# Kernel optimization log

Hardware: AMD Instinct MI355X
Metric: run time of the kernel (lower is better)

Reference implementation:

```python
import jax, jax.numpy as jnp
import numpy as np

N_EMBD = 2560
N_HEAD = 32
HEAD_DIM = N_EMBD // N_HEAD  # 80
ROTARY_DIM = 32
SEQ = 2048
BSZ = 1


def _rope_tables(seq_len, rotary_dim, base=10000.0):
    inv_freq = 1.0 / (base ** (np.arange(0, rotary_dim, 2, dtype=np.float32) / rotary_dim))
    t = np.arange(seq_len, dtype=np.float32)
    freqs = np.outer(t, inv_freq)                      # [S, rd/2]
    emb = np.concatenate([freqs, freqs], axis=-1)      # [S, rd]
    return jnp.asarray(np.cos(emb)), jnp.asarray(np.sin(emb))


def setup_inputs() -> dict:
    key = jax.random.key(0)
    k1, k2, k3, k4, k5 = jax.random.split(key, 5)
    op_size = HEAD_DIM * (N_HEAD + 2 * N_HEAD)  # fused q,k,v => 3*n_embd
    hidden_states = jax.random.normal(k1, (BSZ, SEQ, N_EMBD), dtype=jnp.float32)
    Wqkv_w = jax.random.normal(k2, (op_size, N_EMBD), dtype=jnp.float32) * 0.02
    Wqkv_b = jax.random.normal(k3, (op_size,), dtype=jnp.float32) * 0.02
    out_w = jax.random.normal(k4, (N_EMBD, N_EMBD), dtype=jnp.float32) * 0.02
    out_b = jax.random.normal(k5, (N_EMBD,), dtype=jnp.float32) * 0.02
    cos, sin = _rope_tables(SEQ, ROTARY_DIM)
    return {"hidden_states": hidden_states, "Wqkv_w": Wqkv_w, "Wqkv_b": Wqkv_b,
            "out_w": out_w, "out_b": out_b, "cos": cos, "sin": sin}


def apply_partial_rotary(x, cos, sin):
    # x: [S, B, H, D]; cos/sin: [S, rd]
    rd = cos.shape[-1]
    c = cos[:, None, None, :]
    s = sin[:, None, None, :]
    x_rot = x[..., :rd]
    # NOTE: faithful to source -- rotated half is concatenated WITHOUT negation
    tmp = jnp.concatenate([x[..., rd // 2:rd], x[..., :rd // 2]], axis=-1)
    rotten = x_rot * c + tmp * s
    return jnp.concatenate([rotten, x[..., rd:]], axis=-1)


def reference(hidden_states, Wqkv_w, Wqkv_b, out_w, out_b, cos, sin):
    bsz, q_len, _ = hidden_states.shape
    qkv = hidden_states @ Wqkv_w.T + Wqkv_b            # [B, S, 3*E]
    q, k, v = jnp.split(qkv, 3, axis=-1)
    # [B, S, H, D] -> [S, B, H, D] for rotary
    q = q.reshape(bsz, q_len, N_HEAD, HEAD_DIM).transpose(1, 0, 2, 3)
    k = k.reshape(bsz, q_len, N_HEAD, HEAD_DIM).transpose(1, 0, 2, 3)
    v = v.reshape(bsz, q_len, N_HEAD, HEAD_DIM).transpose(0, 2, 1, 3)  # [B, H, S, D]
    cos_t, sin_t = cos[:q_len], sin[:q_len]
    q = apply_partial_rotary(q, cos_t, sin_t).transpose(1, 2, 0, 3)    # [B, H, S, D]
    k = apply_partial_rotary(k, cos_t, sin_t).transpose(1, 2, 0, 3)    # [B, H, S, D]
    scale = 1.0 / jnp.sqrt(jnp.asarray(HEAD_DIM, dtype=q.dtype))
    scores = jnp.einsum('bhqd,bhkd->bhqk', q, k) * scale
    causal = jnp.tril(jnp.ones((q_len, q_len), dtype=bool))
    scores = jnp.where(causal, scores, jnp.asarray(-1e30, dtype=scores.dtype))
    probs = jax.nn.softmax(scores, axis=-1)
    out = jnp.einsum('bhqk,bhkd->bhqd', probs, v)       # [B, H, S, D]
    out = out.transpose(0, 2, 1, 3).reshape(bsz, q_len, N_EMBD)
    return out @ out_w.T + out_b
```

## Files before the change

### kernel.cpp

```cpp
#include <hip/hip_runtime.h>
#include <cstdint>
#include <cstddef>

typedef unsigned short bf16_t;
typedef __attribute__((ext_vector_type(8))) short bf16x8;
typedef __attribute__((ext_vector_type(4))) float f32x4;

__device__ __forceinline__ float bf2f(bf16_t b) {
  unsigned int u = ((unsigned int)b) << 16;
  return __builtin_bit_cast(float, u);
}
__device__ __forceinline__ bf16_t f2bf(float f) {
  unsigned int u = __builtin_bit_cast(unsigned int, f);
  u += 0x7fffu + ((u >> 16) & 1u);
  return (bf16_t)(u >> 16);
}
__device__ __forceinline__ float lo16(unsigned int u) { return __builtin_bit_cast(float, u << 16); }
__device__ __forceinline__ float hi16(unsigned int u) { return __builtin_bit_cast(float, u & 0xffff0000u); }

constexpr int SEQ = 2048, NE = 2560, NH = 32, HD = 80, OP = 7680;

__global__ void cvt_f32_bf16(const float* __restrict__ s, bf16_t* __restrict__ d) {
  const int t = blockIdx.x * 256 + threadIdx.x;
  float4 v = ((const float4*)s)[t];
  ushort4 o;
  o.x = f2bf(v.x); o.y = f2bf(v.y); o.z = f2bf(v.z); o.w = f2bf(v.w);
  ((ushort4*)d)[t] = o;
}

__device__ __forceinline__ void store_out(bf16_t* p, float v) { *p = f2bf(v); }
__device__ __forceinline__ void store_out(float* p, float v)  { *p = v; }

template <typename OutT>
__global__ __launch_bounds__(256, 2) void gemm_bt_bias(
    const bf16_t* __restrict__ A,
    const bf16_t* __restrict__ B,
    const float*  __restrict__ bias,
    OutT* __restrict__ C,
    int M, int N, int K)
{
  __shared__ bf16_t As[128 * 32];
  __shared__ bf16_t Bs[128 * 32];

  const int tid  = threadIdx.x;
  const int lane = tid & 63;
  const int wave = tid >> 6;
  const int m0 = blockIdx.y * 128;
  const int n0 = blockIdx.x * 128;
  const int mw = (wave >> 1) * 64;
  const int nw = (wave & 1) * 64;
  const int lm = lane & 15;
  const int lq = lane >> 4;

  f32x4 acc[4][4];
#pragma unroll
  for (int i = 0; i < 4; ++i)
#pragma unroll
    for (int j = 0; j < 4; ++j)
      acc[i][j] = (f32x4){0.f, 0.f, 0.f, 0.f};

  const int ldr = lane >> 2;
  const int ldc = (lane & 3) * 8;

  for (int kt = 0; kt < K; kt += 32) {
#pragma unroll
    for (int r = 0; r < 2; ++r) {
      const int seg = wave * 2 + r;
      const int row = seg * 16 + ldr;
      const bf16_t* ga = A + (size_t)(m0 + row) * K + kt + ldc;
      const bf16_t* gb = B + (size_t)(n0 + row) * K + kt + ldc;
      __builtin_amdgcn_global_load_lds(
          (const __attribute__((address_space(1))) unsigned int*)ga,
          (__attribute__((address_space(3))) unsigned int*)&As[seg * 512], 16, 0, 0);
      __builtin_amdgcn_global_load_lds(
          (const __attribute__((address_space(1))) unsigned int*)gb,
          (__attribute__((address_space(3))) unsigned int*)&Bs[seg * 512], 16, 0, 0);
    }
    __syncthreads();

    bf16x8 af[4], bfq[4];
#pragma unroll
    for (int i = 0; i < 4; ++i)
      af[i] = *(const bf16x8*)&As[(mw + i * 16 + lm) * 32 + lq * 8];
#pragma unroll
    for (int j = 0; j < 4; ++j)
      bfq[j] = *(const bf16x8*)&Bs[(nw + j * 16 + lm) * 32 + lq * 8];

#pragma unroll
    for (int i = 0; i < 4; ++i)
#pragma unroll
      for (int j = 0; j < 4; ++j)
        acc[i][j] = __builtin_amdgcn_mfma_f32_16x16x32_bf16(af[i], bfq[j], acc[i][j], 0, 0, 0);

    __syncthreads();
  }

#pragma unroll
  for (int i = 0; i < 4; ++i) {
#pragma unroll
    for (int j = 0; j < 4; ++j) {
      const int n = n0 + nw + j * 16 + lm;
      const float bv = bias[n];
#pragma unroll
      for (int r = 0; r < 4; ++r) {
        const int m = m0 + mw + i * 16 + lq * 4 + r;
        store_out(&C[(size_t)m * N + n], acc[i][j][r] + bv);
      }
    }
  }
}

__global__ void rope_kernel(bf16_t* __restrict__ qkv,
                            const float* __restrict__ cosb,
                            const float* __restrict__ sinb)
{
  const int t = blockIdx.x * 256 + threadIdx.x;
  const int i  = t & 15;
  const int qk = (t >> 4) & 1;
  const int h  = (t >> 5) & 31;
  const int s  = t >> 10;
  const size_t base = (size_t)s * OP + qk * NE + h * HD;
  const float xi = bf2f(qkv[base + i]);
  const float xj = bf2f(qkv[base + i + 16]);
  const float c1 = cosb[s * 32 + i];
  const float s1 = sinb[s * 32 + i];
  const float c2 = cosb[s * 32 + i + 16];
  const float s2 = sinb[s * 32 + i + 16];
  qkv[base + i]      = f2bf(xi * c1 + xj * s1);
  qkv[base + i + 16] = f2bf(xj * c2 + xi * s2);
}

constexpr int KSTR = 96;
constexpr int VSTR = 72;
constexpr int PSTR = 72;

__global__ __launch_bounds__(256, 2) void attn_mfma(
    const bf16_t* __restrict__ qkv, bf16_t* __restrict__ aout)
{
  __shared__ bf16_t Ks[64 * KSTR];
  __shared__ bf16_t Vt[80 * VSTR];
  __shared__ bf16_t Ps[4][32 * PSTR];

  const int h    = blockIdx.y;
  const int qt   = (int)gridDim.x - 1 - blockIdx.x;
  const int q0   = qt * 128;
  const int tid  = threadIdx.x;
  const int lane = tid & 63;
  const int wave = tid >> 6;
  const int lm   = lane & 15;
  const int quad = lane >> 4;

  const int jb0 = 16 * wave;
  const int jb1 = 64 + 16 * wave;
  const int qg0 = q0 + jb0 + lm;
  const int qg1 = q0 + jb1 + lm;

  const int koff = NE + h * HD;
  const int voff = 2 * NE + h * HD;
  const float SC = 0.1118033988749895f;

  bf16x8 qf[2][3];
  {
    const bf16_t* q_r0 = qkv + (size_t)qg0 * OP + h * HD;
    const bf16_t* q_r1 = qkv + (size_t)qg1 * OP + h * HD;
#pragma unroll
    for (int ks = 0; ks < 3; ++ks) {
      const int col = ks * 32 + quad * 8;
      if (col < 80) {
        qf[0][ks] = *(const bf16x8*)(q_r0 + col);
        qf[1][ks] = *(const bf16x8*)(q_r1 + col);
      } else {
        qf[0][ks] = (bf16x8){0,0,0,0,0,0,0,0};
        qf[1][ks] = (bf16x8){0,0,0,0,0,0,0,0};
      }
    }
  }

  int kofs[3];
#pragma unroll
  for (int r = 0; r < 3; ++r) {
    const int e = (wave * 3 + r) * 512 + lane * 8;
    const int row = e / 96, c = e % 96;
    kofs[r] = row * OP + (c < 80 ? c : c - 16);
  }

  const int vp = tid & 31;
  const int vg = tid >> 5;

  f32x4 oacc[5][2];
#pragma unroll
  for (int mt = 0; mt < 5; ++mt) {
    oacc[mt][0] = (f32x4){0.f,0.f,0.f,0.f};
    oacc[mt][1] = (f32x4){0.f,0.f,0.f,0.f};
  }
  float lsum0 = 0.f, lsum1 = 0.f;

  const int ntiles = 2 * qt + 2;
  for (int t = 0; t < ntiles; ++t) {
    const int kb = t * 64;

#pragma unroll
    for (int r = 0; r < 3; ++r) {
      const bf16_t* g = qkv + (size_t)kb * OP + koff + kofs[r];
      __builtin_amdgcn_global_load_lds(
          (const __attribute__((address_space(1))) unsigned int*)g,
          (__attribute__((address_space(3))) unsigned int*)&Ks[(wave * 3 + r) * 512],
          16, 0, 0);
    }
    {
      const bf16_t* va = qkv + (size_t)(kb + 2 * vp) * OP + voff + vg * 10;
      const bf16_t* vb = va + OP;
      unsigned int wa[5], wb[5];
#pragma unroll
      for (int j = 0; j < 5; ++j) {
        wa[j] = *(const unsigned int*)(va + 2 * j);
        wb[j] = *(const unsigned int*)(vb + 2 * j);
      }
#pragma unroll
      for (int tt = 0; tt < 10; ++tt) {
        const unsigned int A = wa[tt >> 1], B = wb[tt >> 1];
        const unsigned int pk = (tt & 1) ? ((A >> 16) | (B & 0xffff0000u))
                                         : ((A & 0xffffu) | (B << 16));
        *(unsigned int*)&Vt[(vg * 10 + tt) * VSTR + 2 * vp] = pk;
      }
    }
    __syncthreads();

    f32x4 sacc[4][2];
#pragma unroll
    for (int mt = 0; mt < 4; ++mt) {
      sacc[mt][0] = (f32x4){0.f,0.f,0.f,0.f};
      sacc[mt][1] = (f32x4){0.f,0.f,0.f,0.f};
    }
#pragma unroll
    for (int ks = 0; ks < 3; ++ks) {
      bf16x8 kf[4];
#pragma unroll
      for (int mt = 0; mt < 4; ++mt)
        kf[mt] = *(const bf16x8*)&Ks[(mt * 16 + lm) * KSTR + ks * 32 + quad * 8];
#pragma unroll
      for (int mt = 0; mt < 4; ++mt) {
        sacc[mt][0] = __builtin_amdgcn_mfma_f32_16x16x32_bf16(kf[mt], qf[0][ks], sacc[mt][0], 0, 0, 0);
        sacc[mt][1] = __builtin_amdgcn_mfma_f32_16x16x32_bf16(kf[mt], qf[1][ks], sacc[mt][1], 0, 0, 0);
      }
    }

    const int keyb = kb + quad * 4;
#pragma unroll
    for (int mt = 0; mt < 4; ++mt) {
#pragma unroll
      for (int nt = 0; nt < 2; ++nt) {
        const int qg = nt ? qg1 : qg0;
        float ps[4];
#pragma unroll
        for (int r = 0; r < 4; ++r) {
          float p = __expf(sacc[mt][nt][r] * SC);
          p = (keyb + mt * 16 + r > qg) ? 0.f : p;
          ps[r] = p;
        }
        if (nt == 0) lsum0 += (ps[0] + ps[1]) + (ps[2] + ps[3]);
        else         lsum1 += (ps[0] + ps[1]) + (ps[2] + ps[3]);
        ushort4 pk;
        pk.x = f2bf(ps[0]); pk.y = f2bf(ps[1]); pk.z = f2bf(ps[2]); pk.w = f2bf(ps[3]);
        *(ushort4*)&Ps[wave][((nt ? jb1 - 64 + 16 : jb0) , (nt * 16 + lm)) * 0 + (nt * 16 + lm) * PSTR + mt * 16 + quad * 4] = pk;
      }
    }

#pragma unroll
    for (int ks = 0; ks < 2; ++ks) {
      bf16x8 vf[5], pf0, pf1;
#pragma unroll
      for (int mt = 0; mt < 5; ++mt)
        vf[mt] = *(const bf16x8*)&Vt[(mt * 16 + lm) * VSTR + ks * 32 + quad * 8];
      pf0 = *(const bf16x8*)&Ps[wave][(0 * 16 + lm) * PSTR + ks * 32 + quad * 8];
      pf1 = *(const bf16x8*)&Ps[wave][(1 * 16 + lm) * PSTR + ks * 32 + quad * 8];
#pragma unroll
      for (int mt = 0; mt < 5; ++mt) {
        oacc[mt][0] = __builtin_amdgcn_mfma_f32_16x16x32_bf16(vf[mt], pf0, oacc[mt][0], 0, 0, 0);
        oacc[mt][1] = __builtin_amdgcn_mfma_f32_16x16x32_bf16(vf[mt], pf1, oacc[mt][1], 0, 0, 0);
      }
    }
    __syncthreads();
  }

  lsum0 += __shfl_xor(lsum0, 16); lsum0 += __shfl_xor(lsum0, 32);
  lsum1 += __shfl_xor(lsum1, 16); lsum1 += __shfl_xor(lsum1, 32);
  const float inv0 = 1.f / lsum0, inv1 = 1.f / lsum1;
#pragma unroll
  for (int nt = 0; nt < 2; ++nt) {
    const int qrow = nt ? qg1 : qg0;
    const float inv = nt ? inv1 : inv0;
    bf16_t* base = aout + (size_t)qrow * NE + h * HD + quad * 4;
#pragma unroll
    for (int mt = 0; mt < 5; ++mt) {
      ushort4 st;
      st.x = f2bf(oacc[mt][nt][0] * inv);
      st.y = f2bf(oacc[mt][nt][1] * inv);
      st.z = f2bf(oacc[mt][nt][2] * inv);
      st.w = f2bf(oacc[mt][nt][3] * inv);
      *(ushort4*)(base + mt * 16) = st;
    }
  }
}

extern "C" void kernel_launch(void* const* d_in, const int* in_sizes, int n_in,
                              void* d_out, int out_size, void* d_ws, size_t ws_size,
                              hipStream_t stream)
{
  const float* hs   = (const float*)d_in[0];
  const float* wqkv = (const float*)d_in[1];
  const float* bqkv = (const float*)d_in[2];
  const float* wout = (const float*)d_in[3];
  const float* bout = (const float*)d_in[4];
  const float* cosb = (const float*)d_in[5];
  const float* sinb = (const float*)d_in[6];

  bf16_t* hs_bf   = (bf16_t*)d_ws;
  bf16_t* wqkv_bf = hs_bf   + (size_t)SEQ * NE;
  bf16_t* wout_bf = wqkv_bf + (size_t)OP * NE;
  bf16_t* qkv     = wout_bf + (size_t)NE * NE;
  bf16_t* aout    = qkv     + (size_t)SEQ * OP;
  float*  out     = (float*)d_out;

  cvt_f32_bf16<<<(SEQ * NE) / 1024, 256, 0, stream>>>(hs,   hs_bf);
  cvt_f32_bf16<<<(OP * NE)  / 1024, 256, 0, stream>>>(wqkv, wqkv_bf);
  cvt_f32_bf16<<<(NE * NE)  / 1024, 256, 0, stream>>>(wout, wout_bf);

  gemm_bt_bias<bf16_t><<<dim3(OP / 128, SEQ / 128), 256, 0, stream>>>(
      hs_bf, wqkv_bf, bqkv, qkv, SEQ, OP, NE);
  rope_kernel<<<(SEQ * NH * 2 * 16) / 256, 256, 0, stream>>>(qkv, cosb, sinb);
  attn_mfma<<<dim3(SEQ / 128, NH), 256, 0, stream>>>(qkv, aout);
  gemm_bt_bias<float><<<dim3(NE / 128, SEQ / 128), 256, 0, stream>>>(
      aout, wout_bf, bout, out, SEQ, NE, NE);
}
```

Baseline: 432.5 us.

## Pad GEMM and attention LDS tiles, merge conversion kernels, raise GEMM occupancy

The GEMM shared-memory tiles get a padded row stride of 40, and the async global-to-LDS loads are remapped to fill that padded layout, with half the waves loading A and half loading B. The goal is to cut LDS bank conflicts on the MFMA fragment reads. GEMM launch bounds go from 2 to 3 blocks per SM. The attention K tile stride is padded to 104 with a matching load remap, and the three fp32-to-bf16 conversion launches become one kernel. The padded layouts rely on the tricky load-to-LDS address mapping, and the extra padding columns are filled with duplicate data.

```diff
diff --git a/kernel.cpp b/kernel.cpp
--- a/kernel.cpp
+++ b/kernel.cpp
@@ -15,13 +15,19 @@
   u += 0x7fffu + ((u >> 16) & 1u);
   return (bf16_t)(u >> 16);
 }
-__device__ __forceinline__ float lo16(unsigned int u) { return __builtin_bit_cast(float, u << 16); }
-__device__ __forceinline__ float hi16(unsigned int u) { return __builtin_bit_cast(float, u & 0xffff0000u); }
 
 constexpr int SEQ = 2048, NE = 2560, NH = 32, HD = 80, OP = 7680;
 
-__global__ void cvt_f32_bf16(const float* __restrict__ s, bf16_t* __restrict__ d) {
-  const int t = blockIdx.x * 256 + threadIdx.x;
+__global__ void cvt3(const float* __restrict__ s0, const float* __restrict__ s1,
+                     const float* __restrict__ s2, bf16_t* __restrict__ d0,
+                     bf16_t* __restrict__ d1, bf16_t* __restrict__ d2)
+{
+  constexpr int N0 = SEQ * NE / 4, N1 = OP * NE / 4, N2 = NE * NE / 4;
+  int t = blockIdx.x * 256 + threadIdx.x;
+  const float* s; bf16_t* d;
+  if (t < N0)            { s = s0; d = d0; }
+  else if (t < N0 + N1)  { s = s1; d = d1; t -= N0; }
+  else                   { s = s2; d = d2; t -= N0 + N1; }
   float4 v = ((const float4*)s)[t];
   ushort4 o;
   o.x = f2bf(v.x); o.y = f2bf(v.y); o.z = f2bf(v.z); o.w = f2bf(v.w);
@@ -31,16 +37,18 @@
 __device__ __forceinline__ void store_out(bf16_t* p, float v) { *p = f2bf(v); }
 __device__ __forceinline__ void store_out(float* p, float v)  { *p = v; }
 
+constexpr int GSTR = 40;
+
 template <typename OutT>
-__global__ __launch_bounds__(256, 2) void gemm_bt_bias(
+__global__ __launch_bounds__(256, 3) void gemm_bt_bias(
     const bf16_t* __restrict__ A,
     const bf16_t* __restrict__ B,
     const float*  __restrict__ bias,
     OutT* __restrict__ C,
     int M, int N, int K)
 {
-  __shared__ bf16_t As[128 * 32];
-  __shared__ bf16_t Bs[128 * 32];
+  __shared__ bf16_t As[128 * GSTR];
+  __shared__ bf16_t Bs[128 * GSTR];
 
   const int tid  = threadIdx.x;
   const int lane = tid & 63;
@@ -59,32 +67,38 @@
     for (int j = 0; j < 4; ++j)
       acc[i][j] = (f32x4){0.f, 0.f, 0.f, 0.f};
 
-  const int ldr = lane >> 2;
-  const int ldc = (lane & 3) * 8;
+  const bf16_t* gsrc = (wave < 2) ? A : B;
+  bf16_t* lbase      = (wave < 2) ? As : Bs;
+  const size_t rowbase = (size_t)((wave < 2) ? m0 : n0) * K;
+  int gofs[5], lofs[5];
+#pragma unroll
+  for (int r = 0; r < 5; ++r) {
+    const int ci  = (wave & 1) * 5 + r;
+    const int c   = ci * 64 + lane;
+    const int row = c / 5;
+    const int cc  = c % 5;
+    const int col = (cc < 4) ? cc * 8 : 0;
+    gofs[r] = row * K + col;
+    lofs[r] = ci * 512;
+  }
 
   for (int kt = 0; kt < K; kt += 32) {
 #pragma unroll
-    for (int r = 0; r < 2; ++r) {
-      const int seg = wave * 2 + r;
-      const int row = seg * 16 + ldr;
-      const bf16_t* ga = A + (size_t)(m0 + row) * K + kt + ldc;
-      const bf16_t* gb = B + (size_t)(n0 + row) * K + kt + ldc;
+    for (int r = 0; r < 5; ++r) {
+      const bf16_t* g = gsrc + rowbase + kt + gofs[r];
       __builtin_amdgcn_global_load_lds(
-          (const __attribute__((address_space(1))) unsigned int*)ga,
-          (__attribute__((address_space(3))) unsigned int*)&As[seg * 512], 16, 0, 0);
-      __builtin_amdgcn_global_load_lds(
-          (const __attribute__((address_space(1))) unsigned int*)gb,
-          (__attribute__((address_space(3))) unsigned int*)&Bs[seg * 512], 16, 0, 0);
+          (const __attribute__((address_space(1))) unsigned int*)g,
+          (__attribute__((address_space(3))) unsigned int*)&lbase[lofs[r]], 16, 0, 0);
     }
     __syncthreads();
 
     bf16x8 af[4], bfq[4];
 #pragma unroll
     for (int i = 0; i < 4; ++i)
-      af[i] = *(const bf16x8*)&As[(mw + i * 16 + lm) * 32 + lq * 8];
+      af[i] = *(const bf16x8*)&As[(mw + i * 16 + lm) * GSTR + lq * 8];
 #pragma unroll
     for (int j = 0; j < 4; ++j)
-      bfq[j] = *(const bf16x8*)&Bs[(nw + j * 16 + lm) * 32 + lq * 8];
+      bfq[j] = *(const bf16x8*)&Bs[(nw + j * 16 + lm) * GSTR + lq * 8];
 
 #pragma unroll
     for (int i = 0; i < 4; ++i)
@@ -130,7 +144,7 @@
   qkv[base + i + 16] = f2bf(xj * c2 + xi * s2);
 }
 
-constexpr int KSTR = 96;
+constexpr int KSTR = 104;
 constexpr int VSTR = 72;
 constexpr int PSTR = 72;
 
@@ -176,12 +190,18 @@
     }
   }
 
-  int kofs[3];
-#pragma unroll
-  for (int r = 0; r < 3; ++r) {
-    const int e = (wave * 3 + r) * 512 + lane * 8;
-    const int row = e / 96, c = e % 96;
-    kofs[r] = row * OP + (c < 80 ? c : c - 16);
+  int kofs[4], klds[4];
+  bool kact[4];
+#pragma unroll
+  for (int r = 0; r < 4; ++r) {
+    const int seg = wave * 4 + r;
+    kact[r] = (seg < 13);
+    const int c   = (seg < 13 ? seg : 0) * 64 + lane;
+    const int row = c / 13;
+    const int cc  = c % 13;
+    const int col = (cc < 10) ? cc * 8 : (cc - 10) * 8;
+    kofs[r] = row * OP + col;
+    klds[r] = (seg < 13 ? seg : 0) * 512;
   }
 
   const int vp = tid & 31;
@@ -200,12 +220,13 @@
     const int kb = t * 64;
 
 #pragma unroll
-    for (int r = 0; r < 3; ++r) {
-      const bf16_t* g = qkv + (size_t)kb * OP + koff + kofs[r];
-      __builtin_amdgcn_global_load_lds(
-          (const __attribute__((address_space(1))) unsigned int*)g,
-          (__attribute__((address_space(3))) unsigned int*)&Ks[(wave * 3 + r) * 512],
-          16, 0, 0);
+    for (int r = 0; r < 4; ++r) {
+      if (kact[r]) {
+        const bf16_t* g = qkv + (size_t)kb * OP + koff + kofs[r];
+        __builtin_amdgcn_global_load_lds(
+            (const __attribute__((address_space(1))) unsigned int*)g,
+            (__attribute__((address_space(3))) unsigned int*)&Ks[klds[r]], 16, 0, 0);
+      }
     }
     {
       const bf16_t* va = qkv + (size_t)(kb + 2 * vp) * OP + voff + vg * 10;
@@ -262,7 +283,7 @@
         else         lsum1 += (ps[0] + ps[1]) + (ps[2] + ps[3]);
         ushort4 pk;
         pk.x = f2bf(ps[0]); pk.y = f2bf(ps[1]); pk.z = f2bf(ps[2]); pk.w = f2bf(ps[3]);
-        *(ushort4*)&Ps[wave][((nt ? jb1 - 64 + 16 : jb0) , (nt * 16 + lm)) * 0 + (nt * 16 + lm) * PSTR + mt * 16 + quad * 4] = pk;
+        *(ushort4*)&Ps[wave][(nt * 16 + lm) * PSTR + mt * 16 + quad * 4] = pk;
       }
     }
 
@@ -322,9 +343,8 @@
   bf16_t* aout    = qkv     + (size_t)SEQ * OP;
   float*  out     = (float*)d_out;
 
-  cvt_f32_bf16<<<(SEQ * NE) / 1024, 256, 0, stream>>>(hs,   hs_bf);
-  cvt_f32_bf16<<<(OP * NE)  / 1024, 256, 0, stream>>>(wqkv, wqkv_bf);
-  cvt_f32_bf16<<<(NE * NE)  / 1024, 256, 0, stream>>>(wout, wout_bf);
+  constexpr int CVT_T = (SEQ * NE + OP * NE + NE * NE) / 4;
+  cvt3<<<CVT_T / 256, 256, 0, stream>>>(hs, wqkv, wout, hs_bf, wqkv_bf, wout_bf);
 
   gemm_bt_bias<bf16_t><<<dim3(OP / 128, SEQ / 128), 256, 0, stream>>>(
       hs_bf, wqkv_bf, bqkv, qkv, SEQ, OP, NE);
```

After: 440.3 us. No clear change (+1.8%).

## Halve attention query tile to 64 rows and merge conversion launches

Applied to the files above, without the earlier changes.

The attention kernel now gives each block 64 query rows instead of 128, so each wave handles one 16-row query fragment. That doubles the grid, cuts register and LDS use, and raises the occupancy hint to 4 blocks per CU. The intent is better occupancy and load balance across the causal triangle, at the cost of loading each K/V tile twice as often per head. The three f32-to-bf16 conversion kernels are also merged into one launch to cut launch overhead.

```diff
diff --git a/kernel.cpp b/kernel.cpp
--- a/kernel.cpp
+++ b/kernel.cpp
@@ -15,13 +15,19 @@
   u += 0x7fffu + ((u >> 16) & 1u);
   return (bf16_t)(u >> 16);
 }
-__device__ __forceinline__ float lo16(unsigned int u) { return __builtin_bit_cast(float, u << 16); }
-__device__ __forceinline__ float hi16(unsigned int u) { return __builtin_bit_cast(float, u & 0xffff0000u); }
 
 constexpr int SEQ = 2048, NE = 2560, NH = 32, HD = 80, OP = 7680;
 
-__global__ void cvt_f32_bf16(const float* __restrict__ s, bf16_t* __restrict__ d) {
-  const int t = blockIdx.x * 256 + threadIdx.x;
+__global__ void cvt3(const float* __restrict__ s0, const float* __restrict__ s1,
+                     const float* __restrict__ s2, bf16_t* __restrict__ d0,
+                     bf16_t* __restrict__ d1, bf16_t* __restrict__ d2)
+{
+  constexpr int N0 = SEQ * NE / 4, N1 = OP * NE / 4;
+  int t = blockIdx.x * 256 + threadIdx.x;
+  const float* s; bf16_t* d;
+  if (t < N0)            { s = s0; d = d0; }
+  else if (t < N0 + N1)  { s = s1; d = d1; t -= N0; }
+  else                   { s = s2; d = d2; t -= N0 + N1; }
   float4 v = ((const float4*)s)[t];
   ushort4 o;
   o.x = f2bf(v.x); o.y = f2bf(v.y); o.z = f2bf(v.z); o.w = f2bf(v.w);
@@ -134,45 +140,36 @@
 constexpr int VSTR = 72;
 constexpr int PSTR = 72;
 
-__global__ __launch_bounds__(256, 2) void attn_mfma(
+__global__ __launch_bounds__(256, 4) void attn_mfma(
     const bf16_t* __restrict__ qkv, bf16_t* __restrict__ aout)
 {
   __shared__ bf16_t Ks[64 * KSTR];
   __shared__ bf16_t Vt[80 * VSTR];
-  __shared__ bf16_t Ps[4][32 * PSTR];
+  __shared__ bf16_t Ps[4][16 * PSTR];
 
   const int h    = blockIdx.y;
   const int qt   = (int)gridDim.x - 1 - blockIdx.x;
-  const int q0   = qt * 128;
+  const int q0   = qt * 64;
   const int tid  = threadIdx.x;
   const int lane = tid & 63;
   const int wave = tid >> 6;
   const int lm   = lane & 15;
   const int quad = lane >> 4;
 
-  const int jb0 = 16 * wave;
-  const int jb1 = 64 + 16 * wave;
-  const int qg0 = q0 + jb0 + lm;
-  const int qg1 = q0 + jb1 + lm;
+  const int qg = q0 + 16 * wave + lm;
 
   const int koff = NE + h * HD;
   const int voff = 2 * NE + h * HD;
   const float SC = 0.1118033988749895f;
 
-  bf16x8 qf[2][3];
+  bf16x8 qf[3];
   {
-    const bf16_t* q_r0 = qkv + (size_t)qg0 * OP + h * HD;
-    const bf16_t* q_r1 = qkv + (size_t)qg1 * OP + h * HD;
+    const bf16_t* q_r = qkv + (size_t)qg * OP + h * HD;
 #pragma unroll
     for (int ks = 0; ks < 3; ++ks) {
       const int col = ks * 32 + quad * 8;
-      if (col < 80) {
-        qf[0][ks] = *(const bf16x8*)(q_r0 + col);
-        qf[1][ks] = *(const bf16x8*)(q_r1 + col);
-      } else {
-        qf[0][ks] = (bf16x8){0,0,0,0,0,0,0,0};
-        qf[1][ks] = (bf16x8){0,0,0,0,0,0,0,0};
-      }
+      if (col < 80) qf[ks] = *(const bf16x8*)(q_r + col);
+      else          qf[ks] = (bf16x8){0,0,0,0,0,0,0,0};
     }
   }
 
@@ -187,15 +184,12 @@
   const int vp = tid & 31;
   const int vg = tid >> 5;
 
-  f32x4 oacc[5][2];
-#pragma unroll
-  for (int mt = 0; mt < 5; ++mt) {
-    oacc[mt][0] = (f32x4){0.f,0.f,0.f,0.f};
-    oacc[mt][1] = (f32x4){0.f,0.f,0.f,0.f};
-  }
-  float lsum0 = 0.f, lsum1 = 0.f;
-
-  const int ntiles = 2 * qt + 2;
+  f32x4 oacc[5];
+#pragma unroll
+  for (int mt = 0; mt < 5; ++mt) oacc[mt] = (f32x4){0.f,0.f,0.f,0.f};
+  float lsum = 0.f;
+
+  const int ntiles = qt + 1;
   for (int t = 0; t < ntiles; ++t) {
     const int kb = t * 64;
 
@@ -226,12 +220,9 @@
     }
     __syncthreads();
 
-    f32x4 sacc[4][2];
-#pragma unroll
-    for (int mt = 0; mt < 4; ++mt) {
-      sacc[mt][0] = (f32x4){0.f,0.f,0.f,0.f};
-      sacc[mt][1] = (f32x4){0.f,0.f,0.f,0.f};
-    }
+    f32x4 sacc[4];
+#pragma unroll
+    for (int mt = 0; mt < 4; ++mt) sacc[mt] = (f32x4){0.f,0.f,0.f,0.f};
 #pragma unroll
     for (int ks = 0; ks < 3; ++ks) {
       bf16x8 kf[4];
@@ -239,67 +230,52 @@
       for (int mt = 0; mt < 4; ++mt)
         kf[mt] = *(const bf16x8*)&Ks[(mt * 16 + lm) * KSTR + ks * 32 + quad * 8];
 #pragma unroll
-      for (int mt = 0; mt < 4; ++mt) {
-        sacc[mt][0] = __builtin_amdgcn_mfma_f32_16x16x32_bf16(kf[mt], qf[0][ks], sacc[mt][0], 0, 0, 0);
-        sacc[mt][1] = __builtin_amdgcn_mfma_f32_16x16x32_bf16(kf[mt], qf[1][ks], sacc[mt][1], 0, 0, 0);
+      for (int mt = 0; mt < 4; ++mt)
+        sacc[mt] = __builtin_amdgcn_mfma_f32_16x16x32_bf16(kf[mt], qf[ks], sacc[mt], 0, 0, 0);
+    }
+
+    const int keyb = kb + quad * 4;
+#pragma unroll
+    for (int mt = 0; mt < 4; ++mt) {
+      float ps[4];
+#pragma unroll
+      for (int r = 0; r < 4; ++r) {
+        float p = __expf(sacc[mt][r] * SC);
+        p = (keyb + mt * 16 + r > qg) ? 0.f : p;
+        ps[r] = p;
       }
-    }
-
-    const int keyb = kb + quad * 4;
-#pragma unroll
-    for (int mt = 0; mt < 4; ++mt) {
-#pragma unroll
-      for (int nt = 0; nt < 2; ++nt) {
-        const int qg = nt ? qg1 : qg0;
-        float ps[4];
-#pragma unroll
-        for (int r = 0; r < 4; ++r) {
-          float p = __expf(sacc[mt][nt][r] * SC);
-          p = (keyb + mt * 16 + r > qg) ? 0.f : p;
-          ps[r] = p;
-        }
-        if (nt == 0) lsum0 += (ps[0] + ps[1]) + (ps[2] + ps[3]);
-        else         lsum1 += (ps[0] + ps[1]) + (ps[2] + ps[3]);
-        ushort4 pk;
-        pk.x = f2bf(ps[0]); pk.y = f2bf(ps[1]); pk.z = f2bf(ps[2]); pk.w = f2bf(ps[3]);
-        *(ushort4*)&Ps[wave][((nt ? jb1 - 64 + 16 : jb0) , (nt * 16 + lm)) * 0 + (nt * 16 + lm) * PSTR + mt * 16 + quad * 4] = pk;
-      }
+      lsum += (ps[0] + ps[1]) + (ps[2] + ps[3]);
+      ushort4 pk;
+      pk.x = f2bf(ps[0]); pk.y = f2bf(ps[1]); pk.z = f2bf(ps[2]); pk.w = f2bf(ps[3]);
+      *(ushort4*)&Ps[wave][lm * PSTR + mt * 16 + quad * 4] = pk;
     }
 
 #pragma unroll
     for (int ks = 0; ks < 2; ++ks) {
-      bf16x8 vf[5], pf0, pf1;
+      bf16x8 vf[5], pf;
 #pragma unroll
       for (int mt = 0; mt < 5; ++mt)
         vf[mt] = *(const bf16x8*)&Vt[(mt * 16 + lm) * VSTR + ks * 32 + quad * 8];
-      pf0 = *(const bf16x8*)&Ps[wave][(0 * 16 + lm) * PSTR + ks * 32 + quad * 8];
-      pf1 = *(const bf16x8*)&Ps[wave][(1 * 16 + lm) * PSTR + ks * 32 + quad * 8];
-#pragma unroll
-      for (int mt = 0; mt < 5; ++mt) {
-        oacc[mt][0] = __builtin_amdgcn_mfma_f32_16x16x32_bf16(vf[mt], pf0, oacc[mt][0], 0, 0, 0);
-        oacc[mt][1] = __builtin_amdgcn_mfma_f32_16x16x32_bf16(vf[mt], pf1, oacc[mt][1], 0, 0, 0);
-      }
+      pf = *(const bf16x8*)&Ps[wave][lm * PSTR + ks * 32 + quad * 8];
+#pragma unroll
+      for (int mt = 0; mt < 5; ++mt)
+        oacc[mt] = __builtin_amdgcn_mfma_f32_16x16x32_bf16(vf[mt], pf, oacc[mt], 0, 0, 0);
     }
     __syncthreads();
   }
 
-  lsum0 += __shfl_xor(lsum0, 16); lsum0 += __shfl_xor(lsum0, 32);
-  lsum1 += __shfl_xor(lsum1, 16); lsum1 += __shfl_xor(lsum1, 32);
-  const float inv0 = 1.f / lsum0, inv1 = 1.f / lsum1;
-#pragma unroll
-  for (int nt = 0; nt < 2; ++nt) {
-    const int qrow = nt ? qg1 : qg0;
-    const float inv = nt ? inv1 : inv0;
-    bf16_t* base = aout + (size_t)qrow * NE + h * HD + quad * 4;
-#pragma unroll
-    for (int mt = 0; mt < 5; ++mt) {
-      ushort4 st;
-      st.x = f2bf(oacc[mt][nt][0] * inv);
-      st.y = f2bf(oacc[mt][nt][1] * inv);
-      st.z = f2bf(oacc[mt][nt][2] * inv);
-      st.w = f2bf(oacc[mt][nt][3] * inv);
-      *(ushort4*)(base + mt * 16) = st;
-    }
+  lsum += __shfl_xor(lsum, 16);
+  lsum += __shfl_xor(lsum, 32);
+  const float inv = 1.f / lsum;
+  bf16_t* base = aout + (size_t)qg * NE + h * HD + quad * 4;
+#pragma unroll
+  for (int mt = 0; mt < 5; ++mt) {
+    ushort4 st;
+    st.x = f2bf(oacc[mt][0] * inv);
+    st.y = f2bf(oacc[mt][1] * inv);
+    st.z = f2bf(oacc[mt][2] * inv);
+    st.w = f2bf(oacc[mt][3] * inv);
+    *(ushort4*)(base + mt * 16) = st;
   }
 }
 
@@ -322,14 +298,13 @@
   bf16_t* aout    = qkv     + (size_t)SEQ * OP;
   float*  out     = (float*)d_out;
 
-  cvt_f32_bf16<<<(SEQ * NE) / 1024, 256, 0, stream>>>(hs,   hs_bf);
-  cvt_f32_bf16<<<(OP * NE)  / 1024, 256, 0, stream>>>(wqkv, wqkv_bf);
-  cvt_f32_bf16<<<(NE * NE)  / 1024, 256, 0, stream>>>(wout, wout_bf);
+  constexpr int CVT_T = (SEQ * NE + OP * NE + NE * NE) / 4;
+  cvt3<<<CVT_T / 256, 256, 0, stream>>>(hs, wqkv, wout, hs_bf, wqkv_bf, wout_bf);
 
   gemm_bt_bias<bf16_t><<<dim3(OP / 128, SEQ / 128), 256, 0, stream>>>(
       hs_bf, wqkv_bf, bqkv, qkv, SEQ, OP, NE);
   rope_kernel<<<(SEQ * NH * 2 * 16) / 256, 256, 0, stream>>>(qkv, cosb, sinb);
-  attn_mfma<<<dim3(SEQ / 128, NH), 256, 0, stream>>>(qkv, aout);
+  attn_mfma<<<dim3(SEQ / 64, NH), 256, 0, stream>>>(qkv, aout);
   gemm_bt_bias<float><<<dim3(NE / 128, SEQ / 128), 256, 0, stream>>>(
       aout, wout_bf, bout, out, SEQ, NE, NE);
 }
```

Result: no change. 434.5 us (+0.5%).
